# Optimization experiments

Measured on AMD Instinct MI355X. Metric: run time of the kernel, lower is better.

## Reference

```python
import jax, jax.numpy as jnp
import numpy as np
from jax import lax

NUM_HEADS = 8
EPS = 1e-12  # torch F.normalize default eps


def setup_inputs() -> dict:
    key = jax.random.key(0)
    ks = jax.random.split(key, 7)
    B, C, H, W = 4, 128, 256, 256
    d = C // 2  # per-branch channels = 64
    x = jax.random.normal(ks[0], (B, C, H, W), jnp.float32)
    w_qkv1 = jax.random.normal(ks[1], (3 * d, d), jnp.float32) * 0.05
    w_qkv2 = jax.random.normal(ks[2], (3 * d, d), jnp.float32) * 0.05
    w_dw1 = jax.random.normal(ks[3], (3 * d, 1, 3, 3), jnp.float32) * 0.05
    w_dw2 = jax.random.normal(ks[4], (3 * d, 1, 3, 3), jnp.float32) * 0.05
    w_po1 = jax.random.normal(ks[5], (d, d), jnp.float32) * 0.05
    w_po2 = jax.random.normal(ks[6], (d, d), jnp.float32) * 0.05
    t1 = jnp.ones((NUM_HEADS, 1, 1), jnp.float32)
    t2 = jnp.ones((NUM_HEADS, 1, 1), jnp.float32)
    return {"x": x, "w_qkv1": w_qkv1, "w_qkv2": w_qkv2, "w_dw1": w_dw1,
            "w_dw2": w_dw2, "w_po1": w_po1, "w_po2": w_po2, "t1": t1, "t2": t2}


def _qkv(xb, w1x1, wdw):
    # 1x1 conv (pointwise) then 3x3 depthwise conv, no bias
    y = jnp.einsum('bchw,oc->bohw', xb, w1x1)
    y = lax.conv_general_dilated(
        y, wdw, window_strides=(1, 1), padding='SAME',
        dimension_numbers=('NCHW', 'OIHW', 'NCHW'),
        feature_group_count=y.shape[1])
    return y


def _heads(t, b, h, w):
    # b (head c) h w -> b head c (h*w)
    return t.reshape(b, NUM_HEADS, -1, h * w)


def _l2norm(t):
    n = jnp.sqrt(jnp.sum(t * t, axis=-1, keepdims=True))
    return t / jnp.maximum(n, EPS)


def reference(x, w_qkv1, w_qkv2, w_dw1, w_dw2, w_po1, w_po2, t1, t2):
    b, c, h, w = x.shape
    x1, x2 = jnp.split(x, 2, axis=1)
    q1, k1, v1 = jnp.split(_qkv(x1, w_qkv1, w_dw1), 3, axis=1)
    q2, k2, v2 = jnp.split(_qkv(x2, w_qkv2, w_dw2), 3, axis=1)
    q1, k1, v1 = (_heads(t, b, h, w) for t in (q1, k1, v1))
    q2, k2, v2 = (_heads(t, b, h, w) for t in (q2, k2, v2))
    q1, k1 = _l2norm(q1), _l2norm(k1)
    q2, k2 = _l2norm(q2), _l2norm(k2)
    # channel-wise attention: [b, head, c_h, c_h]
    attn1 = jax.nn.softmax(jnp.einsum('bhcn,bhdn->bhcd', q1, k1) * t1[None], axis=-1)
    attn2 = jax.nn.softmax(jnp.einsum('bhcn,bhdn->bhcd', q2, k2) * t2[None], axis=-1)
    # cross-branch V swap
    out1 = jnp.einsum('bhcd,bhdn->bhcn', attn1, v2).reshape(b, c // 2, h, w)
    out2 = jnp.einsum('bhcd,bhdn->bhcn', attn2, v1).reshape(b, c // 2, h, w)
    out1 = jnp.einsum('bchw,oc->bohw', out1, w_po1)
    out2 = jnp.einsum('bchw,oc->bohw', out2, w_po2)
    return jnp.concatenate([out1, out2], axis=1)
```

## Files before the change

kernel.cpp:

```cpp
#include <hip/hip_runtime.h>
#include <hip/hip_fp16.h>

#define NPIX 65536
#define WIMG 256
#define HIMG 256
#define TW 16
#define TH 8
#define HSTR 24
#define NSLOT 240
#define YSW 104

typedef __attribute__((ext_vector_type(8))) _Float16 half8;
typedef __attribute__((ext_vector_type(4))) float f32x4;

__device__ __forceinline__ unsigned int h2u(__half2 h) {
  union { __half2 h; unsigned int u; } c; c.h = h; return c.u;
}
__device__ __forceinline__ __half2 u2h(unsigned int u) {
  union { unsigned int u; __half2 h; } c; c.u = u; return c.h;
}
__device__ __forceinline__ __half2 sp2(_Float16 s) {
  union { _Float16 h[2]; __half2 v; } u; u.h[0] = s; u.h[1] = s; return u.v;
}
__device__ __forceinline__ int qk_idx(int ch, int pxblk) {
  return ch * 128 + ((pxblk ^ (ch & 7)) << 3);
}
__device__ __forceinline__ void ld16_lds(const void* g, void* l) {
  __builtin_amdgcn_global_load_lds(
      (const __attribute__((address_space(1))) unsigned int*)g,
      (__attribute__((address_space(3))) unsigned int*)l, 16, 0, 0);
}

__global__ __launch_bounds__(256)
void k_prep(const float* __restrict__ wq1, const float* __restrict__ wq2,
            const float* __restrict__ wd1, const float* __restrict__ wd2,
            float* __restrict__ zbuf,
            _Float16* __restrict__ wqh, _Float16* __restrict__ wdh) {
  int i = blockIdx.x * 256 + threadIdx.x;
  if (i < 6144) {
    zbuf[i] = 0.0f;
  } else {
    int j = i - 6144;
    if (j < 24576) {
      int br = j / 12288, r = j - br * 12288;
      wqh[j] = (_Float16)((br ? wq2 : wq1)[r]);
    } else {
      int k = j - 24576;
      int br = k / 3072, r = k - br * 3072;
      int o = r >> 4, t = r & 15;
      wdh[k] = (t < 9) ? (_Float16)((br ? wd2 : wd1)[o * 9 + t]) : (_Float16)0.0f;
    }
  }
}

__global__ __launch_bounds__(256)
void k_xt(const float* __restrict__ x, __half* __restrict__ xT) {
  __shared__ _Float16 tile[64 * 257];
  const int strip = blockIdx.x;
  const int br = blockIdx.y, b = blockIdx.z;
  const int tid = threadIdx.x;
  const float* xb = x + ((size_t)b * 128 + br * 64) * NPIX + strip * 256;
  #pragma unroll 8
  for (int c = 0; c < 64; ++c)
    tile[c * 257 + tid] = (_Float16)xb[(size_t)c * NPIX + tid];
  __syncthreads();
  __half* xo = xT + ((size_t)(b * 2 + br) * NPIX + strip * 256) * 64;
  const int j = tid & 7;
  #pragma unroll
  for (int i = 0; i < 8; ++i) {
    int p = (tid >> 3) + i * 32;
    half8 h;
    #pragma unroll
    for (int k = 0; k < 8; ++k) h[k] = tile[(j * 8 + k) * 257 + p];
    *(half8*)((_Float16*)xo + p * 64 + j * 8) = h;
  }
}

__global__ __launch_bounds__(256, 3)
void k_qkv(const __half* __restrict__ xT,
           const _Float16* __restrict__ wqh, const _Float16* __restrict__ wdh,
           const float* __restrict__ zpage,
           __half* __restrict__ vbuf, float* __restrict__ gram,
           float* __restrict__ sqq, float* __restrict__ sqk)
{
  __shared__ __align__(16) _Float16 xs[256 * 64];
  __shared__ __align__(16) _Float16 ys[4 * 16 * YSW];

  const int tid = threadIdx.x;
  const int lane = tid & 63;
  const int wid = tid >> 6;
  const int tile = blockIdx.x;
  const int br = blockIdx.y;
  const int b = blockIdx.z;
  const int tx0 = (tile & 15) * TW;
  const int ty0 = (tile >> 4) * TH;

  const _Float16* wqb = wqh + br * 12288;
  const _Float16* wdb = wdh + br * 3072;
  const __half* xTimg = xT + (size_t)(b * 2 + br) * NPIX * 64;

  {
    const int j = lane & 7, pl = lane >> 3;
    for (int it = wid; it < 30; it += 4) {
      int s = it * 8;
      int slot = s + pl;
      int hy = slot / HSTR;
      int hx = slot - hy * HSTR;
      int gy = ty0 - 1 + hy, gx = tx0 - 1 + hx;
      bool valid = (hx < 18) && ((unsigned)gy < HIMG) && ((unsigned)gx < WIMG);
      const void* src = valid
        ? (const void*)((const _Float16*)xTimg + (size_t)(gy * WIMG + gx) * 64
                        + ((j ^ (slot & 7)) << 3))
        : (const void*)((const char*)zpage + lane * 16);
      ld16_lds(src, (void*)(xs + s * 64));
    }
  }
  asm volatile("s_waitcnt vmcnt(0)" ::: "memory");
  __syncthreads();

  const int col = lane & 15;
  const int qrow = lane >> 4;
  const int dc = lane >> 2;
  const int rr = (lane >> 1) & 1;
  const int dhalf = lane & 1;

  _Float16* ysw = ys + wid * (16 * YSW);
  unsigned int qreg[4][4], kreg[4][4];

#define PW16(P_, G_) do {                                                     \
    const _Float16* wp_ = wqb + ((((P_) * 64 + (G_) * 16 + col) << 6) + qrow * 8); \
    half8 wf0_ = *(const half8*)(wp_);                                        \
    half8 wf1_ = *(const half8*)(wp_ + 32);                                   \
    _Pragma("unroll")                                                         \
    for (int j = 0; j < 6; ++j) {                                             \
      int px = wid * 48 + j * 16 + col;                                       \
      half8 af0 = *(const half8*)(xs + px * 64 + (((qrow    ) ^ (px & 7)) << 3)); \
      half8 af1 = *(const half8*)(xs + px * 64 + (((4 + qrow) ^ (px & 7)) << 3)); \
      f32x4 a0 = {0,0,0,0};                                                   \
      a0 = __builtin_amdgcn_mfma_f32_16x16x32_f16(af0, wf0_, a0, 0, 0, 0);    \
      a0 = __builtin_amdgcn_mfma_f32_16x16x32_f16(af1, wf1_, a0, 0, 0, 0);    \
      uint2 s_ = {h2u(__floats2half2_rn(a0[0], a0[1])),                       \
                  h2u(__floats2half2_rn(a0[2], a0[3]))};                      \
      *(uint2*)(ysw + col * YSW + j * 16 + qrow * 4) = s_;                    \
    }                                                                         \
  } while (0)

#define DW16(P_, G_) do {                                                     \
    const int o_ = (G_) * 16 + dc;                                            \
    const _Float16* wdp_ = wdb + (((P_) * 64 + o_) << 4);                     \
    half8 wv_ = *(const half8*)wdp_;                                          \
    _Float16 w8_ = wdp_[8];                                                   \
    __half2 w2_[9];                                                           \
    _Pragma("unroll")                                                         \
    for (int j = 0; j < 8; ++j) w2_[j] = sp2(wv_[j]);                         \
    w2_[8] = sp2(w8_);                                                        \
    __half2 a_[4];                                                            \
    _Pragma("unroll")                                                         \
    for (int k2 = 0; k2 < 4; ++k2) a_[k2] = u2h(0u);                          \
    _Pragma("unroll")                                                         \
    for (int ky = 0; ky < 3; ++ky) {                                          \
      const _Float16* rp_ = ysw + dc * YSW + (rr + ky) * HSTR + dhalf * 8;    \
      uint2 ra_ = *(const uint2*)rp_;                                         \
      uint2 rb_ = *(const uint2*)(rp_ + 4);                                   \
      unsigned int rc_ = *(const unsigned int*)(rp_ + 8);                     \
      unsigned int W_[5] = {ra_.x, ra_.y, rb_.x, rb_.y, rc_};                 \
      _Pragma("unroll")                                                       \
      for (int k2 = 0; k2 < 4; ++k2) {                                        \
        unsigned int M_ = (W_[k2] >> 16) | (W_[k2 + 1] << 16);                \
        a_[k2] = __hfma2(w2_[ky * 3 + 0], u2h(W_[k2]), a_[k2]);               \
        a_[k2] = __hfma2(w2_[ky * 3 + 1], u2h(M_), a_[k2]);                   \
        a_[k2] = __hfma2(w2_[ky * 3 + 2], u2h(W_[k2 + 1]), a_[k2]);           \
      }                                                                       \
    }                                                                         \
    if ((P_) == 0) {                                                          \
      _Pragma("unroll")                                                       \
      for (int k2 = 0; k2 < 4; ++k2) qreg[G_][k2] = h2u(a_[k2]);              \
    } else if ((P_) == 1) {                                                   \
      _Pragma("unroll")                                                       \
      for (int k2 = 0; k2 < 4; ++k2) kreg[G_][k2] = h2u(a_[k2]);              \
    } else {                                                                  \
      __half* vrow_ = (__half*)(vbuf                                          \
          + ((size_t)((br * 4 + b) * 64 + o_)) * NPIX                         \
          + (ty0 + wid * 2 + rr) * WIMG + tx0 + dhalf * 8);                   \
      uint4 s_ = {h2u(a_[0]), h2u(a_[1]), h2u(a_[2]), h2u(a_[3])};            \
      *(uint4*)vrow_ = s_;                                                    \
    }                                                                         \
  } while (0)

  PW16(2, 0); DW16(2, 0); PW16(2, 1); DW16(2, 1);
  PW16(2, 2); DW16(2, 2); PW16(2, 3); DW16(2, 3);
  PW16(0, 0); DW16(0, 0); PW16(0, 1); DW16(0, 1);
  PW16(0, 2); DW16(0, 2); PW16(0, 3); DW16(0, 3);
  PW16(1, 0); DW16(1, 0); PW16(1, 1); DW16(1, 1);
  PW16(1, 2); DW16(1, 2); PW16(1, 3); DW16(1, 3);

  __syncthreads();
  {
    _Float16* qsb = xs;
    _Float16* ksb = xs + 64 * 128;
    const int pb = wid * 4 + rr * 2 + dhalf;
    #pragma unroll
    for (int g = 0; g < 4; ++g) {
      int ch = g * 16 + dc;
      uint4 q_ = {qreg[g][0], qreg[g][1], qreg[g][2], qreg[g][3]};
      uint4 k_ = {kreg[g][0], kreg[g][1], kreg[g][2], kreg[g][3]};
      *(uint4*)(qsb + qk_idx(ch, pb)) = q_;
      *(uint4*)(ksb + qk_idx(ch, pb)) = k_;
    }
  }
  __syncthreads();

  {
    const _Float16* qsb = xs;
    const _Float16* ksb = xs + 64 * 128;
    f32x4 gqk = {0,0,0,0}, gqq = {0,0,0,0}, gkk = {0,0,0,0};
    int ch = wid * 16 + col;
    #pragma unroll
    for (int kc = 0; kc < 4; ++kc) {
      int pb = kc * 4 + qrow;
      half8 aq = *(const half8*)(qsb + qk_idx(ch, pb));
      half8 bk = *(const half8*)(ksb + qk_idx(ch, pb));
      gqk = __builtin_amdgcn_mfma_f32_16x16x32_f16(aq, bk, gqk, 0, 0, 0);
      gqq = __builtin_amdgcn_mfma_f32_16x16x32_f16(aq, aq, gqq, 0, 0, 0);
      gkk = __builtin_amdgcn_mfma_f32_16x16x32_f16(bk, bk, gkk, 0, 0, 0);
    }
    const int gb_off = (br * 4 + b);
    if (((lane >> 3) & 1) == (lane >> 5)) {
      float* gb = gram + gb_off * 512;
      int kch = ch;
      int qc0 = wid * 16 + qrow * 4;
      #pragma unroll
      for (int r = 0; r < 4; ++r) {
        int qch = qc0 + r;
        atomicAdd(&gb[(qch >> 3) * 64 + (qch & 7) * 8 + (kch & 7)], gqk[r]);
      }
    }
    if ((col >> 2) == qrow) {
      atomicAdd(&sqq[gb_off * 64 + ch], gqq[lane & 3]);
      atomicAdd(&sqk[gb_off * 64 + ch], gkk[lane & 3]);
    }
  }
#undef PW16
#undef DW16
}

__global__ __launch_bounds__(64)
void k_attn(const float* __restrict__ gram, const float* __restrict__ sqq,
            const float* __restrict__ sqk,
            const float* __restrict__ wpo1, const float* __restrict__ wpo2,
            const float* __restrict__ t1, const float* __restrict__ t2,
            _Float16* __restrict__ wefft)
{
  const int br = blockIdx.x, b = blockIdx.y;
  const int t = threadIdx.x;
  __shared__ float attn[8][8][8];
  const float* gb = gram + (br * 4 + b) * 512;
  const float* sq = sqq + (br * 4 + b) * 64;
  const float* sk = sqk + (br * 4 + b) * 64;
  const float* tt = br ? t2 : t1;
  {
    int h = t >> 3, cq = t & 7;
    float ts = tt[h];
    float qn = fmaxf(sqrtf(sq[h * 8 + cq]), 1e-12f);
    float lg[8], m = -1e30f;
    #pragma unroll
    for (int d2 = 0; d2 < 8; ++d2) {
      float kn = fmaxf(sqrtf(sk[h * 8 + d2]), 1e-12f);
      lg[d2] = ts * gb[h * 64 + cq * 8 + d2] / (qn * kn);
      m = fmaxf(m, lg[d2]);
    }
    float s = 0.f;
    #pragma unroll
    for (int d2 = 0; d2 < 8; ++d2) { lg[d2] = expf(lg[d2] - m); s += lg[d2]; }
    float inv = 1.0f / s;
    #pragma unroll
    for (int d2 = 0; d2 < 8; ++d2) attn[h][cq][d2] = lg[d2] * inv;
  }
  __syncthreads();
  const float* wpo = br ? wpo2 : wpo1;
  _Float16* wt = wefft + (br * 4 + b) * 4096;
  for (int cp = 0; cp < 64; ++cp) {
    int hp = cp >> 3, ip = cp & 7;
    float acc = 0.f;
    #pragma unroll
    for (int j = 0; j < 8; ++j)
      acc += wpo[t * 64 + hp * 8 + j] * attn[hp][j][ip];
    wt[t * 64 + cp] = (_Float16)acc;
  }
}

__global__ __launch_bounds__(256)
void k_out(const __half* __restrict__ vbuf, const _Float16* __restrict__ wefft,
           float* __restrict__ out)
{
  __shared__ __align__(16) _Float16 vs[64 * 128];
  __shared__ __align__(16) _Float16 vt[128 * 64];

  const int strip = blockIdx.x;
  const int obr = blockIdx.y, b = blockIdx.z;
  const int brv = 1 - obr;
  const int tid = threadIdx.x;
  const int lane = tid & 63;
  const int wid = tid >> 6;
  const int col = lane & 15;
  const int qrow = lane >> 4;

  const __half* vb = vbuf + ((size_t)(brv * 4 + b) * 64) * NPIX + strip * 128;

  for (int i = 0; i < 4; ++i) {
    int it = wid * 4 + i;
    const void* src = (const void*)((const _Float16*)vb
        + (size_t)(it * 4 + (lane >> 4)) * NPIX + (lane & 15) * 8);
    ld16_lds(src, (void*)(vs + it * 512));
  }
  asm volatile("s_waitcnt vmcnt(0)" ::: "memory");
  __syncthreads();

  {
    int px = tid & 127, cb = tid >> 7;
    #pragma unroll
    for (int j = 0; j < 4; ++j) {
      half8 h;
      #pragma unroll
      for (int e = 0; e < 8; ++e) h[e] = vs[(cb * 32 + j * 8 + e) * 128 + px];
      int chunk = cb * 4 + j;
      *(half8*)(vt + ((px * 8 + (chunk ^ (px & 7))) << 3)) = h;
    }
  }
  __syncthreads();

  const _Float16* wt = wefft + (obr * 4 + b) * 4096;
  half8 bf[2][4];
  #pragma unroll
  for (int nt = 0; nt < 4; ++nt)
    #pragma unroll
    for (int kc = 0; kc < 2; ++kc)
      bf[kc][nt] = *(const half8*)(wt + (nt * 16 + col) * 64 + kc * 32 + qrow * 8);

  float* ob = out + ((size_t)b * 128 + obr * 64) * NPIX + strip * 128;
  #pragma unroll
  for (int mi = 0; mi < 2; ++mi) {
    int mt = wid * 2 + mi;
    int px = mt * 16 + col;
    half8 af0 = *(const half8*)(vt + ((px * 8 + ((qrow    ) ^ (px & 7))) << 3));
    half8 af1 = *(const half8*)(vt + ((px * 8 + ((4 + qrow) ^ (px & 7))) << 3));
    f32x4 acc[4] = {{0,0,0,0},{0,0,0,0},{0,0,0,0},{0,0,0,0}};
    #pragma unroll
    for (int nt = 0; nt < 4; ++nt) {
      acc[nt] = __builtin_amdgcn_mfma_f32_16x16x32_f16(af0, bf[0][nt], acc[nt], 0, 0, 0);
      acc[nt] = __builtin_amdgcn_mfma_f32_16x16x32_f16(af1, bf[1][nt], acc[nt], 0, 0, 0);
    }
    int pxd = mt * 16 + qrow * 4;
    #pragma unroll
    for (int nt = 0; nt < 4; ++nt) {
      float4 s = {acc[nt][0], acc[nt][1], acc[nt][2], acc[nt][3]};
      *(float4*)(ob + (size_t)(nt * 16 + col) * NPIX + pxd) = s;
    }
  }
}

extern "C" void kernel_launch(void* const* d_in, const int* in_sizes, int n_in,
                              void* d_out, int out_size, void* d_ws, size_t ws_size,
                              hipStream_t stream) {
  const float* x     = (const float*)d_in[0];
  const float* wqkv1 = (const float*)d_in[1];
  const float* wqkv2 = (const float*)d_in[2];
  const float* wdw1  = (const float*)d_in[3];
  const float* wdw2  = (const float*)d_in[4];
  const float* wpo1  = (const float*)d_in[5];
  const float* wpo2  = (const float*)d_in[6];
  const float* t1    = (const float*)d_in[7];
  const float* t2    = (const float*)d_in[8];

  char* ws = (char*)d_ws;
  __half* vbuf = (__half*)ws;
  float* gram  = (float*)(ws + 67108864);
  float* sqq   = gram + 4096;
  float* sqk   = sqq + 512;
  float* zpage = sqk + 512;
  _Float16* wqkvh = (_Float16*)(zpage + 1024);
  _Float16* wdwh  = wqkvh + 24576;
  _Float16* wefft = wdwh + 6144;

  __half* xT = (__half*)d_out;

  k_prep<<<dim3(144), dim3(256), 0, stream>>>(wqkv1, wqkv2, wdw1, wdw2,
                                              gram, wqkvh, wdwh);
  k_xt<<<dim3(256, 2, 4), dim3(256), 0, stream>>>(x, xT);
  k_qkv<<<dim3(512, 2, 4), dim3(256), 0, stream>>>(xT, wqkvh, wdwh,
                                                   zpage, vbuf, gram, sqq, sqk);
  k_attn<<<dim3(2, 4), dim3(64), 0, stream>>>(gram, sqq, sqk, wpo1, wpo2, t1, t2, wefft);
  k_out<<<dim3(512, 2, 4), dim3(256), 0, stream>>>(vbuf, wefft, (float*)d_out);
}
```

Before: 224.2 us.

## Share pointwise halo tile across waves in k_qkv instead of per-wave recompute

The 1x1-conv output tile, including its halo, now lives in one block-wide LDS buffer. Its 15 MFMA m-tiles are split across the four waves, so each wave no longer recomputes the overlapping halo rows it needs for the 3x3 depthwise conv. The depthwise stage is remapped so each wave handles 4 channels across all 8 tile rows. This shrinks the LDS footprint, and launch bounds are raised to 4 blocks per SM. In exchange, about 23 block-wide barriers are added between the pointwise and depthwise stages, and the work split is uneven (4/4/4/3 m-tiles).

```diff
diff --git a/kernel.cpp b/kernel.cpp
--- a/kernel.cpp
+++ b/kernel.cpp
@@ -8,7 +8,7 @@
 #define TH 8
 #define HSTR 24
 #define NSLOT 240
-#define YSW 104
+#define YCH 248
 
 typedef __attribute__((ext_vector_type(8))) _Float16 half8;
 typedef __attribute__((ext_vector_type(4))) float f32x4;
@@ -76,7 +76,7 @@
   }
 }
 
-__global__ __launch_bounds__(256, 3)
+__global__ __launch_bounds__(256, 4)
 void k_qkv(const __half* __restrict__ xT,
            const _Float16* __restrict__ wqh, const _Float16* __restrict__ wdh,
            const float* __restrict__ zpage,
@@ -84,7 +84,7 @@
            float* __restrict__ sqq, float* __restrict__ sqk)
 {
   __shared__ __align__(16) _Float16 xs[256 * 64];
-  __shared__ __align__(16) _Float16 ys[4 * 16 * YSW];
+  __shared__ __align__(16) _Float16 ys[16 * YCH];
 
   const int tid = threadIdx.x;
   const int lane = tid & 63;
@@ -120,33 +120,32 @@
 
   const int col = lane & 15;
   const int qrow = lane >> 4;
-  const int dc = lane >> 2;
-  const int rr = (lane >> 1) & 1;
-  const int dhalf = lane & 1;
-
-  _Float16* ysw = ys + wid * (16 * YSW);
+  const int rel = wid * 4 + (lane >> 4);
+  const int row = (lane >> 1) & 7;
+  const int half = lane & 1;
+
   unsigned int qreg[4][4], kreg[4][4];
 
 #define PW16(P_, G_) do {                                                     \
     const _Float16* wp_ = wqb + ((((P_) * 64 + (G_) * 16 + col) << 6) + qrow * 8); \
     half8 wf0_ = *(const half8*)(wp_);                                        \
     half8 wf1_ = *(const half8*)(wp_ + 32);                                   \
-    _Pragma("unroll")                                                         \
-    for (int j = 0; j < 6; ++j) {                                             \
-      int px = wid * 48 + j * 16 + col;                                       \
+    for (int mt = wid; mt < 15; mt += 4) {                                    \
+      int px = mt * 16 + col;                                                 \
       half8 af0 = *(const half8*)(xs + px * 64 + (((qrow    ) ^ (px & 7)) << 3)); \
       half8 af1 = *(const half8*)(xs + px * 64 + (((4 + qrow) ^ (px & 7)) << 3)); \
       f32x4 a0 = {0,0,0,0};                                                   \
       a0 = __builtin_amdgcn_mfma_f32_16x16x32_f16(af0, wf0_, a0, 0, 0, 0);    \
       a0 = __builtin_amdgcn_mfma_f32_16x16x32_f16(af1, wf1_, a0, 0, 0, 0);    \
-      uint2 s_ = {h2u(__floats2half2_rn(a0[0], a0[1])),                       \
-                  h2u(__floats2half2_rn(a0[2], a0[3]))};                      \
-      *(uint2*)(ysw + col * YSW + j * 16 + qrow * 4) = s_;                    \
+      int pxd = mt * 16 + qrow * 4;                                           \
+      uint2 s0_ = {h2u(__floats2half2_rn(a0[0], a0[1])),                      \
+                   h2u(__floats2half2_rn(a0[2], a0[3]))};                     \
+      *(uint2*)(ys + col * YCH + pxd) = s0_;                                  \
     }                                                                         \
   } while (0)
 
 #define DW16(P_, G_) do {                                                     \
-    const int o_ = (G_) * 16 + dc;                                            \
+    const int o_ = (G_) * 16 + rel;                                           \
     const _Float16* wdp_ = wdb + (((P_) * 64 + o_) << 4);                     \
     half8 wv_ = *(const half8*)wdp_;                                          \
     _Float16 w8_ = wdp_[8];                                                   \
@@ -159,7 +158,7 @@
     for (int k2 = 0; k2 < 4; ++k2) a_[k2] = u2h(0u);                          \
     _Pragma("unroll")                                                         \
     for (int ky = 0; ky < 3; ++ky) {                                          \
-      const _Float16* rp_ = ysw + dc * YSW + (rr + ky) * HSTR + dhalf * 8;    \
+      const _Float16* rp_ = ys + rel * YCH + (row + ky) * HSTR + half * 8;    \
       uint2 ra_ = *(const uint2*)rp_;                                         \
       uint2 rb_ = *(const uint2*)(rp_ + 4);                                   \
       unsigned int rc_ = *(const unsigned int*)(rp_ + 8);                     \
@@ -181,27 +180,32 @@
     } else {                                                                  \
       __half* vrow_ = (__half*)(vbuf                                          \
           + ((size_t)((br * 4 + b) * 64 + o_)) * NPIX                         \
-          + (ty0 + wid * 2 + rr) * WIMG + tx0 + dhalf * 8);                   \
+          + (ty0 + row) * WIMG + tx0 + half * 8);                             \
       uint4 s_ = {h2u(a_[0]), h2u(a_[1]), h2u(a_[2]), h2u(a_[3])};            \
       *(uint4*)vrow_ = s_;                                                    \
     }                                                                         \
   } while (0)
 
-  PW16(2, 0); DW16(2, 0); PW16(2, 1); DW16(2, 1);
-  PW16(2, 2); DW16(2, 2); PW16(2, 3); DW16(2, 3);
-  PW16(0, 0); DW16(0, 0); PW16(0, 1); DW16(0, 1);
-  PW16(0, 2); DW16(0, 2); PW16(0, 3); DW16(0, 3);
-  PW16(1, 0); DW16(1, 0); PW16(1, 1); DW16(1, 1);
-  PW16(1, 2); DW16(1, 2); PW16(1, 3); DW16(1, 3);
-
-  __syncthreads();
+  PW16(0, 0); __syncthreads(); DW16(0, 0); __syncthreads();
+  PW16(0, 1); __syncthreads(); DW16(0, 1); __syncthreads();
+  PW16(0, 2); __syncthreads(); DW16(0, 2); __syncthreads();
+  PW16(0, 3); __syncthreads(); DW16(0, 3); __syncthreads();
+  PW16(1, 0); __syncthreads(); DW16(1, 0); __syncthreads();
+  PW16(1, 1); __syncthreads(); DW16(1, 1); __syncthreads();
+  PW16(1, 2); __syncthreads(); DW16(1, 2); __syncthreads();
+  PW16(1, 3); __syncthreads(); DW16(1, 3); __syncthreads();
+  PW16(2, 0); __syncthreads(); DW16(2, 0); __syncthreads();
+  PW16(2, 1); __syncthreads(); DW16(2, 1); __syncthreads();
+  PW16(2, 2); __syncthreads(); DW16(2, 2); __syncthreads();
+  PW16(2, 3); __syncthreads(); DW16(2, 3);
+
   {
     _Float16* qsb = xs;
     _Float16* ksb = xs + 64 * 128;
-    const int pb = wid * 4 + rr * 2 + dhalf;
+    const int pb = row * 2 + half;
     #pragma unroll
     for (int g = 0; g < 4; ++g) {
-      int ch = g * 16 + dc;
+      int ch = g * 16 + rel;
       uint4 q_ = {qreg[g][0], qreg[g][1], qreg[g][2], qreg[g][3]};
       uint4 k_ = {kreg[g][0], kreg[g][1], kreg[g][2], kreg[g][3]};
       *(uint4*)(qsb + qk_idx(ch, pb)) = q_;
```

New measurement: 240.9 us. 7.5% more time.
